# Optimization experiments

Measured on AMD Instinct MI355X. Metric: run time of the kernel, lower is better.

The kernel has to match this reference:

```python
import jax, jax.numpy as jnp
import numpy as np

LATENT = 292
T = 120          # max_length
CHARSET = 35     # charset_length
B = 512
H1, H2, H3 = 701, 701, 901


def _p(key, shape, scale=0.05):
    return jax.random.normal(key, shape, dtype=jnp.float32) * scale


def setup_inputs() -> dict:
    key = jax.random.key(0)
    ks = jax.random.split(key, 12)
    z32 = lambda *s: jnp.zeros(s, jnp.float32)
    return {
        "z": jax.random.normal(ks[0], (B, LATENT), dtype=jnp.float32),
        # linear_1: Dense(latent_dim, selu)
        "W1": _p(ks[1], (LATENT, LATENT)), "b1": z32(LATENT),
        # gru_1 (Keras GRU, reset_after=True): kernel [in,3H], recurrent [H,3H], two bias vectors [3H]
        "gWi1": _p(ks[2], (LATENT, 3 * H1)), "gWh1": _p(ks[3], (H1, 3 * H1)),
        "gbi1": z32(3 * H1), "gbh1": z32(3 * H1),
        # gru_2
        "gWi2": _p(ks[4], (H1, 3 * H2)), "gWh2": _p(ks[5], (H2, 3 * H2)),
        "gbi2": z32(3 * H2), "gbh2": z32(3 * H2),
        # gru_3
        "gWi3": _p(ks[6], (H2, 3 * H3)), "gWh3": _p(ks[7], (H3, 3 * H3)),
        "gbi3": z32(3 * H3), "gbh3": z32(3 * H3),
        # linear_2: TimeDistributed(Dense(charset_length))
        "Wo": _p(ks[8], (H3, CHARSET)), "bo": z32(CHARSET),
    }


def _gru(x_seq, Wi, Wh, bi, bh):
    """Keras GRU (reset_after=True, gate order z,r,h), return_sequences=True.
    x_seq: [B,T,D] -> [B,T,H]. Input projections hoisted out of the scan."""
    H = Wh.shape[0]
    bsz = x_seq.shape[0]
    xp = jnp.einsum('btd,dg->btg', x_seq, Wi) + bi  # [B,T,3H]
    xp = jnp.transpose(xp, (1, 0, 2))               # [T,B,3H] for scan
    h0 = jnp.zeros((bsz, H), x_seq.dtype)

    def step(h, xt):
        rp = h @ Wh + bh                             # recurrent projection [B,3H]
        xz, xr, xh = jnp.split(xt, 3, axis=-1)
        rz, rr, rh = jnp.split(rp, 3, axis=-1)
        zg = jax.nn.sigmoid(xz + rz)
        rg = jax.nn.sigmoid(xr + rr)
        hh = jnp.tanh(xh + rg * rh)                  # reset applied after recurrent matmul
        hn = zg * h + (1.0 - zg) * hh
        return hn, hn

    _, ys = jax.lax.scan(step, h0, xp)               # ys: [T,B,H]
    return jnp.transpose(ys, (1, 0, 2))


def reference(z, W1, b1, gWi1, gWh1, gbi1, gbh1, gWi2, gWh2, gbi2, gbh2,
              gWi3, gWh3, gbi3, gbh3, Wo, bo):
    x = jax.nn.selu(z @ W1 + b1)                             # [B,latent]
    xs = jnp.broadcast_to(x[:, None, :], (x.shape[0], T, x.shape[1]))  # RepeatVector
    h = _gru(xs, gWi1, gWh1, gbi1, gbh1)                     # [B,T,701]
    h = _gru(h, gWi2, gWh2, gbi2, gbh2)                      # [B,T,701] (dropout inactive at inference)
    h = _gru(h, gWi3, gWh3, gbi3, gbh3)                      # [B,T,901]
    logits = jnp.einsum('bth,hc->btc', h, Wo) + bo           # [B,T,charset]
    return jax.nn.softmax(logits, axis=2)
```

## Files before the change

kernel.cpp:

```cpp
#include <hip/hip_runtime.h>
#include <hip/hip_bf16.h>
#include <math.h>

typedef unsigned short u16;
typedef __attribute__((ext_vector_type(4))) float f32x4;
typedef __attribute__((ext_vector_type(8))) short s16x8;

#define BB  512
#define TT  120
#define LAT 292
#define HH1 701
#define HH3 901
#define H1P 704
#define H3P 960
#define CH  35

static const size_t O_X    = 0;
static const size_t O_XP1  = 598016;
static const size_t O_H1F  = 4923392;
static const size_t O_H2F  = 7806976;
static const size_t O_H3F  = 10690560;
static const size_t O_H1B  = 14622720;
static const size_t O_H2B  = 16064512;
static const size_t O_H3B  = 17506304;
static const size_t O_WHT1 = 19472384;
static const size_t O_WIT2 = 22446080;
static const size_t O_WHT2 = 25419776;
static const size_t O_WIT3 = 28393472;
static const size_t O_WHT3 = 32358400;
static const size_t O_WOT  = 37765120;
static const size_t O_TAB  = 37888000;
static const size_t ZERO_BYTES = 14548992;

#define DSWZ(row, g) ((((g) ^ ((row) & 7)) << 4))

static __device__ __forceinline__ u16 f2b(float f){
  union { float f; unsigned int i; } v; v.f = f;
  unsigned int x = v.i;
  return (u16)((x + 0x7FFFu + ((x >> 16) & 1u)) >> 16);
}

#define GLL16(g, l) __builtin_amdgcn_global_load_lds( \
    (const __attribute__((address_space(1))) unsigned int*)(g), \
    (__attribute__((address_space(3))) unsigned int*)(l), 16, 0, 0)

__launch_bounds__(256)
__global__ void k_selu(const float* __restrict__ z, const float* __restrict__ W1,
                       const float* __restrict__ b1, float* __restrict__ x)
{
  int idx = blockIdx.x * 256 + threadIdx.x;
  if (idx >= BB * LAT) return;
  int b = idx / LAT, i = idx - b * LAT;
  float acc = b1[i];
  const float* zr = z + (size_t)b * LAT;
  for (int k = 0; k < LAT; ++k)
    acc += zr[k] * W1[k * LAT + i];
  const float alpha = 1.6732632423543772f, scale = 1.0507009873554805f;
  x[idx] = scale * (acc > 0.f ? acc : alpha * (expf(acc) - 1.f));
}

__launch_bounds__(256)
__global__ void k_xp1(const float* __restrict__ x, const float* __restrict__ Wi1,
                      const float* __restrict__ bi1, float* __restrict__ xp1)
{
  int nb = blockIdx.x % 9, bb = blockIdx.x / 9;
  int n = nb * 256 + threadIdx.x;
  int b0 = bb * 8;
  if (n >= 2112) return;
  if (n >= 2103) { for (int r = 0; r < 8; ++r) xp1[(size_t)(b0 + r) * 2112 + n] = 0.f; return; }
  float bias = bi1[n];
  float acc[8];
  for (int r = 0; r < 8; ++r) acc[r] = bias;
  for (int k = 0; k < LAT; ++k) {
    float w = Wi1[(size_t)k * 2103 + n];
    #pragma unroll
    for (int r = 0; r < 8; ++r) acc[r] += x[(size_t)(b0 + r) * LAT + k] * w;
  }
  for (int r = 0; r < 8; ++r) xp1[(size_t)(b0 + r) * 2112 + n] = acc[r];
}

__launch_bounds__(256)
__global__ void k_transpose(const float* __restrict__ W, u16* __restrict__ WT,
                            int K, int N, int Kpad, int RowsPad)
{
  int tilesN = RowsPad / 64;
  int tk = blockIdx.x / tilesN, tn = blockIdx.x % tilesN;
  int k0 = tk * 64, n0 = tn * 64;
  __shared__ u16 lds[64][72];
  int tid = threadIdx.x;
  int nl = tid & 63, q = tid >> 6;
  for (int i = 0; i < 16; ++i) {
    int kl = q * 16 + i;
    int k = k0 + kl, n = n0 + nl;
    lds[kl][nl] = (k < K && n < N) ? f2b(W[(size_t)k * N + n]) : (u16)0;
  }
  __syncthreads();
  for (int i = 0; i < 16; ++i) {
    int rl = q * 16 + i;
    WT[(size_t)(n0 + rl) * Kpad + k0 + nl] = lds[nl][rl];
  }
}

__global__ void k_maketab(unsigned int* __restrict__ tab)
{
  if (threadIdx.x != 0 || blockIdx.x != 0) return;
  for (int x = 0; x < 8; ++x) {
    for (int li = 0; li < 32; ++li) {
      unsigned v;
      if (li < 15) {
        int t3 = 15 * x + li;
        v = 0xFFFF0000u | (2u << 12) | ((unsigned)(t3 & 7) << 8) | (unsigned)(t3 >> 3);
      } else if (li < 26) {
        int t2 = 11 * x + (li - 15);
        v = 0xFFFF0000u | (1u << 12) | ((unsigned)(t2 & 7) << 8) | (unsigned)(t2 >> 3);
      } else if (li < 31) {
        int pi = 5 * x + (li - 26);
        int i0 = 2 * pi, i1 = 2 * pi + 1;
        unsigned lo = ((unsigned)(i0 & 7) << 8) | (unsigned)(i0 >> 3);
        unsigned hw = ((unsigned)(i1 & 7) << 8) | (unsigned)(i1 >> 3);
        v = lo | (hw << 16);
      } else {
        if (x < 4) {
          unsigned lo = (3u << 12) | ((unsigned)(2 * x) << 8);
          unsigned hw = (3u << 12) | ((unsigned)(2 * x + 1) << 8);
          v = lo | (hw << 16);
        } else {
          int pi = 40 + (x - 4);
          int i0 = 2 * pi, i1 = 2 * pi + 1;
          unsigned lo = ((unsigned)(i0 & 7) << 8) | (unsigned)(i0 >> 3);
          unsigned hw = ((unsigned)(i1 & 7) << 8) | (unsigned)(i1 >> 3);
          v = lo | (hw << 16);
        }
      }
      tab[x + 8 * li] = v;
    }
  }
}


static __device__ __forceinline__ void stage_gru(
    const u16* __restrict__ A, int As, const u16* __restrict__ W, int Ws, int WH,
    int r0, int j0, int kbase, int wl, int lane, char* buf)
{
  #pragma unroll
  for (int i = 0; i < 8; ++i) {
    int slot = wl * 512 + i * 64 + lane;
    const u16* g;
    if (slot < 512) {
      int row = slot >> 3, gl = slot & 7;
      int gq = gl ^ (row & 7);
      g = A + (size_t)(r0 + row) * As + kbase + gq * 8;
    } else {
      int s2 = slot - 512;
      int gate = s2 >> 9, loc = s2 & 511;
      int col = loc >> 3, gl = loc & 7;
      int gq = gl ^ (col & 7);
      g = W + ((size_t)gate * WH + j0 + col) * Ws + kbase + gq * 8;
    }
    char* l = buf + (wl * 512 + i * 64) * 16;
    GLL16(g, l);
  }
}

template<int HACC>
static __device__ __forceinline__ void mm_gru(const char* gb, int wr, int wc, int m16, int kg,
                                              f32x4 (&acc)[4][2][2])
{
  #pragma unroll
  for (int s = 0; s < 2; ++s) {
    s16x8 af[2];
    #pragma unroll
    for (int fm = 0; fm < 2; ++fm) {
      int row = wr * 32 + fm * 16 + m16;
      af[fm] = *(const s16x8*)(gb + row * 128 + DSWZ(row, s * 4 + kg));
    }
    #pragma unroll
    for (int g = 0; g < 3; ++g) {
      #pragma unroll
      for (int fn = 0; fn < 2; ++fn) {
        int col = wc * 32 + fn * 16 + m16;
        s16x8 bf = *(const s16x8*)(gb + 8192 + g * 8192 + col * 128 + DSWZ(col, s * 4 + kg));
        const int ai = (g == 2) ? HACC : g;
        #pragma unroll
        for (int fm = 0; fm < 2; ++fm)
          acc[ai][fm][fn] = __builtin_amdgcn_mfma_f32_16x16x32_bf16(af[fm], bf, acc[ai][fm][fn], 0, 0, 0);
      }
    }
  }
}

static __device__ __forceinline__ void gru_pipe(
    const u16* A0, int As0, const u16* W0, int Ws0,
    const u16* A1, int As1, const u16* W1p, int Ws1,
    int WH, int n0, int n1, int k1off,
    int r0, int j0, char* g0, char* g1, int wl, int lane,
    int wr, int wc, int m16, int kg, f32x4 (&acc)[4][2][2])
{
  const int n = n0 + n1;
#define STG(C, BUF) do { int c_ = (C); \
    if (c_ < n0) stage_gru(A0, As0, W0, Ws0, WH, r0, j0, c_ * 64, wl, lane, (BUF)); \
    else         stage_gru(A1, As1, W1p, Ws1, WH, r0, j0, (c_ - n0) * 64 + k1off, wl, lane, (BUF)); \
  } while (0)
  STG(0, g0);
  __syncthreads();
  for (int ch = 0; ch < n; ch += 2) {
    if (ch + 1 < n) STG(ch + 1, g1);
    if (ch < n0) mm_gru<2>(g0, wr, wc, m16, kg, acc);
    else         mm_gru<3>(g0, wr, wc, m16, kg, acc);
    __syncthreads();
    if (ch + 1 >= n) break;
    if (ch + 2 < n) STG(ch + 2, g0);
    if (ch + 1 < n0) mm_gru<2>(g1, wr, wc, m16, kg, acc);
    else             mm_gru<3>(g1, wr, wc, m16, kg, acc);
    __syncthreads();
  }
#undef STG
}

__launch_bounds__(512, 2)
__global__ void k_wave(int s, const unsigned int* __restrict__ tab,
    const u16* __restrict__ WhT1, const u16* __restrict__ WiT2, const u16* __restrict__ WhT2,
    const u16* __restrict__ WiT3, const u16* __restrict__ WhT3, const u16* __restrict__ WoT,
    const float* __restrict__ xp1,
    const float* __restrict__ gbh1,
    const float* __restrict__ gbi2, const float* __restrict__ gbh2,
    const float* __restrict__ gbi3, const float* __restrict__ gbh3,
    const float* __restrict__ bo,
    float* __restrict__ h1f, u16* __restrict__ h1b,
    float* __restrict__ h2f, u16* __restrict__ h2b,
    float* __restrict__ h3f, u16* __restrict__ h3b,
    float* __restrict__ out)
{
  extern __shared__ __align__(16) char smem[];
  const int tid  = threadIdx.x;
  const int wgrp = tid >> 8;
  const int ltid = tid & 255;
  const int lane = tid & 63;
  const int wl   = (tid >> 6) & 3;
  const int wr = wl >> 1, wc = wl & 1;
  const int m16 = lane & 15, kg = lane >> 4;
  char* g0 = smem + wgrp * 65536;
  char* g1 = g0 + 32768;

  const unsigned e  = tab[blockIdx.x];
  const unsigned lo = e & 0xFFFFu, hi = e >> 16;
  const bool ksplit = (hi == 0xFFFFu);
  const unsigned item = (!ksplit && wgrp == 1) ? hi : lo;
  const int L  = (item >> 12) & 3;
  const int rr = (item >> 8) & 0xF;
  const int cc = item & 0xFF;
  const int t = s - L;
  if (t < 0 || t >= TT) return;
  const int cur = s & 1, prv = cur ^ 1;

  if (L == 3) {
    const int r0 = rr * 64;
    const u16* Ab = h3b + (size_t)prv * BB * H3P;
    f32x4 acc2[2][2];
    { f32x4 z4 = {0.f,0.f,0.f,0.f}; for (int a=0;a<2;++a) for (int b=0;b<2;++b) acc2[a][b]=z4; }
    int4 ra[2], rb2[2];
    const int n = H3P / 64;
    #pragma unroll
    for (int it = 0; it < 2; ++it) {
      int gi = it * 256 + ltid; int r = gi >> 3, gq = gi & 7;
      ra[it]  = *(const int4*)(Ab + (size_t)(r0 + r) * H3P + gq * 8);
      rb2[it] = *(const int4*)(WoT + (size_t)r * H3P + gq * 8);
    }
    #pragma unroll
    for (int it = 0; it < 2; ++it) {
      int gi = it * 256 + ltid; int r = gi >> 3, gq = gi & 7;
      *(int4*)(g0 + r * 128 + DSWZ(r, gq)) = ra[it];
      *(int4*)(g0 + 8192 + r * 128 + DSWZ(r, gq)) = rb2[it];
    }
    __syncthreads();
    for (int ch = 0; ch < n; ++ch) {
      const bool have = (ch + 1 < n);
      if (have) {
        int kb = (ch + 1) * 64;
        #pragma unroll
        for (int it = 0; it < 2; ++it) {
          int gi = it * 256 + ltid; int r = gi >> 3, gq = gi & 7;
          ra[it]  = *(const int4*)(Ab + (size_t)(r0 + r) * H3P + kb + gq * 8);
          rb2[it] = *(const int4*)(WoT + (size_t)r * H3P + kb + gq * 8);
        }
      }
      #pragma unroll
      for (int s2 = 0; s2 < 2; ++s2) {
        s16x8 af[2], bf[2];
        #pragma unroll
        for (int fm = 0; fm < 2; ++fm) {
          int row = wr * 32 + fm * 16 + m16;
          af[fm] = *(const s16x8*)(g0 + row * 128 + DSWZ(row, s2 * 4 + kg));
        }
        #pragma unroll
        for (int fn = 0; fn < 2; ++fn) {
          int col = wc * 32 + fn * 16 + m16;
          bf[fn] = *(const s16x8*)(g0 + 8192 + col * 128 + DSWZ(col, s2 * 4 + kg));
        }
        #pragma unroll
        for (int fm = 0; fm < 2; ++fm)
          #pragma unroll
          for (int fn = 0; fn < 2; ++fn)
            acc2[fm][fn] = __builtin_amdgcn_mfma_f32_16x16x32_bf16(af[fm], bf[fn], acc2[fm][fn], 0, 0, 0);
      }
      if (have) {
        __syncthreads();
        #pragma unroll
        for (int it = 0; it < 2; ++it) {
          int gi = it * 256 + ltid; int r = gi >> 3, gq = gi & 7;
          *(int4*)(g0 + r * 128 + DSWZ(r, gq)) = ra[it];
          *(int4*)(g0 + 8192 + r * 128 + DSWZ(r, gq)) = rb2[it];
        }
        __syncthreads();
      }
    }
    __syncthreads();
    float (*ldsL)[68] = (float (*)[68])g0;
    #pragma unroll
    for (int fn = 0; fn < 2; ++fn) {
      int col = wc * 32 + fn * 16 + m16;
      float bov = (col < CH) ? bo[col] : 0.f;
      #pragma unroll
      for (int fm = 0; fm < 2; ++fm)
        #pragma unroll
        for (int ii = 0; ii < 4; ++ii)
          ldsL[wr * 32 + fm * 16 + kg * 4 + ii][col] = acc2[fm][fn][ii] + bov;
    }
    __syncthreads();
    if (ltid < 64) {
      int b = r0 + ltid;
      float mx = -1e30f;
      for (int c2 = 0; c2 < CH; ++c2) mx = fmaxf(mx, ldsL[ltid][c2]);
      float sum = 0.f;
      for (int c2 = 0; c2 < CH; ++c2) sum += expf(ldsL[ltid][c2] - mx);
      float inv = 1.f / sum;
      size_t ob = ((size_t)b * TT + t) * CH;
      for (int c2 = 0; c2 < CH; ++c2) out[ob + c2] = expf(ldsL[ltid][c2] - mx) * inv;
    }
    return;
  }

  int H, HP;
  const u16 *A0 = nullptr, *W0 = nullptr, *A1 = nullptr, *W1p = nullptr;
  int As0 = 0, Ws0 = 0, As1 = 0, Ws1 = 0, n0 = 0, n1 = 0, k1off = 0;
  const float *bi = nullptr, *bh;
  float *hfP, *hfC; u16 *hbC;
  if (L == 0) {
    H = HH1; HP = H1P;
    A1 = h1b + (size_t)prv * BB * H1P; As1 = H1P; W1p = WhT1; Ws1 = H1P; n1 = 11;
    bh = gbh1;
    hfP = h1f + (size_t)prv * BB * H1P; hfC = h1f + (size_t)cur * BB * H1P;
    hbC = h1b + (size_t)cur * BB * H1P;
  } else if (L == 1) {
    H = HH1; HP = H1P;
    bi = gbi2; bh = gbh2;
    hfP = h2f + (size_t)prv * BB * H1P; hfC = h2f + (size_t)cur * BB * H1P;
    hbC = h2b + (size_t)cur * BB * H1P;
    if (wgrp == 0) { A0 = h1b + (size_t)prv * BB * H1P; As0 = H1P; W0 = WiT2; Ws0 = H1P; n0 = 11; }
    else           { A1 = h2b + (size_t)prv * BB * H1P; As1 = H1P; W1p = WhT2; Ws1 = H1P; n1 = 11; }
  } else {
    H = HH3; HP = H3P;
    bi = gbi3; bh = gbh3;
    hfP = h3f + (size_t)prv * BB * H3P; hfC = h3f + (size_t)cur * BB * H3P;
    hbC = h3b + (size_t)cur * BB * H3P;
    if (wgrp == 0) {
      A0 = h2b + (size_t)prv * BB * H1P; As0 = H1P; W0 = WiT3; Ws0 = H1P; n0 = 11;
      A1 = h3b + (size_t)prv * BB * H3P; As1 = H3P; W1p = WhT3; Ws1 = H3P; n1 = 2; k1off = 0;
    } else {
      A1 = h3b + (size_t)prv * BB * H3P; As1 = H3P; W1p = WhT3; Ws1 = H3P; n1 = 13; k1off = 128;
    }
  }
  const int r0 = rr * 64, j0 = cc * 64;

  f32x4 acc[4][2][2];
  {
    f32x4 z4 = {0.f, 0.f, 0.f, 0.f};
    for (int g = 0; g < 4; ++g) for (int a = 0; a < 2; ++a) for (int b = 0; b < 2; ++b) acc[g][a][b] = z4;
  }

  gru_pipe(A0, As0, W0, Ws0, A1, As1, W1p, Ws1, H, n0, n1, k1off,
           r0, j0, g0, g1, wl, lane, wr, wc, m16, kg, acc);

  if (ksplit) {
    __syncthreads();
    float* red = (float*)smem;
    if (wgrp == 1) {
      float* b = red + ltid * 64;
      #pragma unroll
      for (int g = 0; g < 4; ++g)
        #pragma unroll
        for (int fm = 0; fm < 2; ++fm)
          #pragma unroll
          for (int fn = 0; fn < 2; ++fn)
            *(f32x4*)(b + ((g * 2 + fm) * 2 + fn) * 4) = acc[g][fm][fn];
    }
    __syncthreads();
    if (wgrp == 1) return;
    {
      const float* b = red + ltid * 64;
      #pragma unroll
      for (int g = 0; g < 4; ++g)
        #pragma unroll
        for (int fm = 0; fm < 2; ++fm)
          #pragma unroll
          for (int fn = 0; fn < 2; ++fn)
            acc[g][fm][fn] += *(const f32x4*)(b + ((g * 2 + fm) * 2 + fn) * 4);
    }
  }

  #pragma unroll
  for (int fn = 0; fn < 2; ++fn) {
    int j = j0 + wc * 32 + fn * 16 + m16;
    if (j >= H) continue;
    float bhz = bh[j], bhr = bh[H + j], bhh = bh[2 * H + j];
    float biz = 0.f, bir = 0.f, bih = 0.f;
    if (L != 0) { biz = bi[j]; bir = bi[H + j]; bih = bi[2 * H + j]; }
    #pragma unroll
    for (int fm = 0; fm < 2; ++fm) {
      #pragma unroll
      for (int ii = 0; ii < 4; ++ii) {
        int row = r0 + wr * 32 + fm * 16 + kg * 4 + ii;
        float az  = acc[0][fm][fn][ii];
        float ar  = acc[1][fm][fn][ii];
        float axh = acc[2][fm][fn][ii];
        float arh = acc[3][fm][fn][ii];
        float pz, pr, xh_, rh_;
        if (L == 0) {
          const float* xr_ = xp1 + (size_t)row * 2112;
          pz  = xr_[j] + az + bhz;
          pr  = xr_[HH1 + j] + ar + bhr;
          xh_ = xr_[2 * HH1 + j];
          rh_ = arh + bhh;
        } else {
          pz  = az + biz + bhz;
          pr  = ar + bir + bhr;
          xh_ = axh + bih;
          rh_ = arh + bhh;
        }
        float zg = 1.f / (1.f + expf(-pz));
        float rg = 1.f / (1.f + expf(-pr));
        float hh = tanhf(xh_ + rg * rh_);
        float hp = hfP[(size_t)row * HP + j];
        float hn = zg * hp + (1.f - zg) * hh;
        hfC[(size_t)row * HP + j] = hn;
        hbC[(size_t)row * HP + j] = f2b(hn);
      }
    }
  }
}

extern "C" void kernel_launch(void* const* d_in, const int* in_sizes, int n_in,
                              void* d_out, int out_size, void* d_ws, size_t ws_size,
                              hipStream_t stream)
{
  const float* z    = (const float*)d_in[0];
  const float* W1   = (const float*)d_in[1];
  const float* b1   = (const float*)d_in[2];
  const float* gWi1 = (const float*)d_in[3];
  const float* gWh1 = (const float*)d_in[4];
  const float* gbi1 = (const float*)d_in[5];
  const float* gbh1 = (const float*)d_in[6];
  const float* gWi2 = (const float*)d_in[7];
  const float* gWh2 = (const float*)d_in[8];
  const float* gbi2 = (const float*)d_in[9];
  const float* gbh2 = (const float*)d_in[10];
  const float* gWi3 = (const float*)d_in[11];
  const float* gWh3 = (const float*)d_in[12];
  const float* gbi3 = (const float*)d_in[13];
  const float* gbh3 = (const float*)d_in[14];
  const float* Wo   = (const float*)d_in[15];
  const float* bo   = (const float*)d_in[16];

  char* ws = (char*)d_ws;
  float* x_f  = (float*)(ws + O_X);
  float* xp1  = (float*)(ws + O_XP1);
  float* h1f  = (float*)(ws + O_H1F);
  float* h2f  = (float*)(ws + O_H2F);
  float* h3f  = (float*)(ws + O_H3F);
  u16*   h1b  = (u16*)(ws + O_H1B);
  u16*   h2b  = (u16*)(ws + O_H2B);
  u16*   h3b  = (u16*)(ws + O_H3B);
  u16*   WhT1 = (u16*)(ws + O_WHT1);
  u16*   WiT2 = (u16*)(ws + O_WIT2);
  u16*   WhT2 = (u16*)(ws + O_WHT2);
  u16*   WiT3 = (u16*)(ws + O_WIT3);
  u16*   WhT3 = (u16*)(ws + O_WHT3);
  u16*   WoT  = (u16*)(ws + O_WOT);
  unsigned int* tab = (unsigned int*)(ws + O_TAB);

  hipFuncSetAttribute((const void*)k_wave,
                      hipFuncAttributeMaxDynamicSharedMemorySize, 131072);

  hipMemsetAsync(ws + O_H1F, 0, ZERO_BYTES, stream);

  k_maketab<<<1, 64, 0, stream>>>(tab);
  k_selu<<<(BB * LAT + 255) / 256, 256, 0, stream>>>(z, W1, b1, x_f);
  k_xp1<<<9 * 64, 256, 0, stream>>>(x_f, gWi1, gbi1, xp1);

  k_transpose<<<11 * 33, 256, 0, stream>>>(gWh1, WhT1, 701, 2103, 704, 2112);
  k_transpose<<<11 * 33, 256, 0, stream>>>(gWi2, WiT2, 701, 2103, 704, 2112);
  k_transpose<<<11 * 33, 256, 0, stream>>>(gWh2, WhT2, 701, 2103, 704, 2112);
  k_transpose<<<11 * 44, 256, 0, stream>>>(gWi3, WiT3, 701, 2703, 704, 2816);
  k_transpose<<<15 * 44, 256, 0, stream>>>(gWh3, WhT3, 901, 2703, 960, 2816);
  k_transpose<<<15 * 1, 256, 0, stream>>>(Wo, WoT, 901, 35, 960, 64);

  for (int s = 0; s < TT + 3; ++s)
    k_wave<<<256, 512, 131072, stream>>>(s, tab, WhT1, WiT2, WhT2, WiT3, WhT3, WoT, xp1,
                                         gbh1, gbi2, gbh2, gbi3, gbh3, bo,
                                         h1f, h1b, h2f, h2b, h3f, h3b, (float*)d_out);
}
```

Measured before the change: 4.983 ms.

## Replace double-buffered K=64 staging with 4-slot K=32 ring and vmcnt waits

```diff
diff --git a/kernel.cpp b/kernel.cpp
--- a/kernel.cpp
+++ b/kernel.cpp
@@ -137,84 +137,78 @@
   }
 }
 
-
-static __device__ __forceinline__ void stage_gru(
+#define RD32(base, row, q) ((base) + (row) * 64 + ((((q) - ((row) >> 2)) & 3) << 4))
+
+static __device__ __forceinline__ void stage32(
     const u16* __restrict__ A, int As, const u16* __restrict__ W, int Ws, int WH,
     int r0, int j0, int kbase, int wl, int lane, char* buf)
 {
   #pragma unroll
-  for (int i = 0; i < 8; ++i) {
-    int slot = wl * 512 + i * 64 + lane;
-    const u16* g;
-    if (slot < 512) {
-      int row = slot >> 3, gl = slot & 7;
-      int gq = gl ^ (row & 7);
-      g = A + (size_t)(r0 + row) * As + kbase + gq * 8;
+  for (int i = 0; i < 4; ++i) {
+    const int si = wl * 4 + i;
+    char* l = buf + si * 1024;
+    if (si < 4) {
+      int slot = si * 64 + lane;
+      int row = slot >> 2, gl = slot & 3;
+      int gq = (gl + (row >> 2)) & 3;
+      GLL16(A + (size_t)(r0 + row) * As + kbase + gq * 8, l);
     } else {
-      int s2 = slot - 512;
-      int gate = s2 >> 9, loc = s2 & 511;
-      int col = loc >> 3, gl = loc & 7;
-      int gq = gl ^ (col & 7);
-      g = W + ((size_t)gate * WH + j0 + col) * Ws + kbase + gq * 8;
-    }
-    char* l = buf + (wl * 512 + i * 64) * 16;
-    GLL16(g, l);
+      int s2 = si * 64 + lane - 256;
+      int gate = s2 >> 8, loc = s2 & 255;
+      int col = loc >> 2, gl = loc & 3;
+      int gq = (gl + (col >> 2)) & 3;
+      GLL16(W + ((size_t)gate * WH + j0 + col) * Ws + kbase + gq * 8, l);
+    }
   }
 }
 
 template<int HACC>
-static __device__ __forceinline__ void mm_gru(const char* gb, int wr, int wc, int m16, int kg,
-                                              f32x4 (&acc)[4][2][2])
-{
+static __device__ __forceinline__ void mm32(const char* gb, int wr, int wc, int m16, int kg,
+                                            f32x4 (&acc)[4][2][2])
+{
+  s16x8 af[2];
   #pragma unroll
-  for (int s = 0; s < 2; ++s) {
-    s16x8 af[2];
+  for (int fm = 0; fm < 2; ++fm) {
+    int row = wr * 32 + fm * 16 + m16;
+    af[fm] = *(const s16x8*)RD32(gb, row, kg);
+  }
+  #pragma unroll
+  for (int g = 0; g < 3; ++g) {
     #pragma unroll
-    for (int fm = 0; fm < 2; ++fm) {
-      int row = wr * 32 + fm * 16 + m16;
-      af[fm] = *(const s16x8*)(gb + row * 128 + DSWZ(row, s * 4 + kg));
-    }
-    #pragma unroll
-    for (int g = 0; g < 3; ++g) {
+    for (int fn = 0; fn < 2; ++fn) {
+      int col = wc * 32 + fn * 16 + m16;
+      s16x8 bf = *(const s16x8*)RD32(gb + 4096 + g * 4096, col, kg);
+      const int ai = (g == 2) ? HACC : g;
       #pragma unroll
-      for (int fn = 0; fn < 2; ++fn) {
-        int col = wc * 32 + fn * 16 + m16;
-        s16x8 bf = *(const s16x8*)(gb + 8192 + g * 8192 + col * 128 + DSWZ(col, s * 4 + kg));
-        const int ai = (g == 2) ? HACC : g;
-        #pragma unroll
-        for (int fm = 0; fm < 2; ++fm)
-          acc[ai][fm][fn] = __builtin_amdgcn_mfma_f32_16x16x32_bf16(af[fm], bf, acc[ai][fm][fn], 0, 0, 0);
-      }
-    }
-  }
-}
-
-static __device__ __forceinline__ void gru_pipe(
+      for (int fm = 0; fm < 2; ++fm)
+        acc[ai][fm][fn] = __builtin_amdgcn_mfma_f32_16x16x32_bf16(af[fm], bf, acc[ai][fm][fn], 0, 0, 0);
+    }
+  }
+}
+
+static __device__ __forceinline__ void gru_pipe32(
     const u16* A0, int As0, const u16* W0, int Ws0,
     const u16* A1, int As1, const u16* W1p, int Ws1,
     int WH, int n0, int n1, int k1off,
-    int r0, int j0, char* g0, char* g1, int wl, int lane,
+    int r0, int j0, char* ring, int wl, int lane,
     int wr, int wc, int m16, int kg, f32x4 (&acc)[4][2][2])
 {
   const int n = n0 + n1;
-#define STG(C, BUF) do { int c_ = (C); \
-    if (c_ < n0) stage_gru(A0, As0, W0, Ws0, WH, r0, j0, c_ * 64, wl, lane, (BUF)); \
-    else         stage_gru(A1, As1, W1p, Ws1, WH, r0, j0, (c_ - n0) * 64 + k1off, wl, lane, (BUF)); \
+#define STG32(C) do { int c_ = (C); char* b_ = ring + (c_ & 3) * 16384; \
+    if (c_ < n0) stage32(A0, As0, W0, Ws0, WH, r0, j0, c_ * 32, wl, lane, b_); \
+    else         stage32(A1, As1, W1p, Ws1, WH, r0, j0, (c_ - n0) * 32 + k1off, wl, lane, b_); \
   } while (0)
-  STG(0, g0);
-  __syncthreads();
-  for (int ch = 0; ch < n; ch += 2) {
-    if (ch + 1 < n) STG(ch + 1, g1);
-    if (ch < n0) mm_gru<2>(g0, wr, wc, m16, kg, acc);
-    else         mm_gru<3>(g0, wr, wc, m16, kg, acc);
-    __syncthreads();
-    if (ch + 1 >= n) break;
-    if (ch + 2 < n) STG(ch + 2, g0);
-    if (ch + 1 < n0) mm_gru<2>(g1, wr, wc, m16, kg, acc);
-    else             mm_gru<3>(g1, wr, wc, m16, kg, acc);
-    __syncthreads();
-  }
-#undef STG
+  STG32(0); STG32(1); STG32(2);
+  for (int ch = 0; ch < n; ++ch) {
+    if (ch + 2 < n)      asm volatile("s_waitcnt vmcnt(8)" ::: "memory");
+    else if (ch + 1 < n) asm volatile("s_waitcnt vmcnt(4)" ::: "memory");
+    else                 asm volatile("s_waitcnt vmcnt(0)" ::: "memory");
+    __builtin_amdgcn_s_barrier();
+    if (ch + 3 < n) STG32(ch + 3);
+    if (ch < n0) mm32<2>(ring + (ch & 3) * 16384, wr, wc, m16, kg, acc);
+    else         mm32<3>(ring + (ch & 3) * 16384, wr, wc, m16, kg, acc);
+  }
+#undef STG32
 }
 
 __launch_bounds__(512, 2)
@@ -239,8 +233,7 @@
   const int wl   = (tid >> 6) & 3;
   const int wr = wl >> 1, wc = wl & 1;
   const int m16 = lane & 15, kg = lane >> 4;
-  char* g0 = smem + wgrp * 65536;
-  char* g1 = g0 + 32768;
+  char* ring = smem + wgrp * 65536;
 
   const unsigned e  = tab[blockIdx.x];
   const unsigned lo = e & 0xFFFFu, hi = e >> 16;
@@ -254,6 +247,7 @@
   const int cur = s & 1, prv = cur ^ 1;
 
   if (L == 3) {
+    char* g0 = ring;
     const int r0 = rr * 64;
     const u16* Ab = h3b + (size_t)prv * BB * H3P;
     f32x4 acc2[2][2];
@@ -347,7 +341,7 @@
   float *hfP, *hfC; u16 *hbC;
   if (L == 0) {
     H = HH1; HP = H1P;
-    A1 = h1b + (size_t)prv * BB * H1P; As1 = H1P; W1p = WhT1; Ws1 = H1P; n1 = 11;
+    A1 = h1b + (size_t)prv * BB * H1P; As1 = H1P; W1p = WhT1; Ws1 = H1P; n1 = 22;
     bh = gbh1;
     hfP = h1f + (size_t)prv * BB * H1P; hfC = h1f + (size_t)cur * BB * H1P;
     hbC = h1b + (size_t)cur * BB * H1P;
@@ -356,18 +350,18 @@
     bi = gbi2; bh = gbh2;
     hfP = h2f + (size_t)prv * BB * H1P; hfC = h2f + (size_t)cur * BB * H1P;
     hbC = h2b + (size_t)cur * BB * H1P;
-    if (wgrp == 0) { A0 = h1b + (size_t)prv * BB * H1P; As0 = H1P; W0 = WiT2; Ws0 = H1P; n0 = 11; }
-    else           { A1 = h2b + (size_t)prv * BB * H1P; As1 = H1P; W1p = WhT2; Ws1 = H1P; n1 = 11; }
+    if (wgrp == 0) { A0 = h1b + (size_t)prv * BB * H1P; As0 = H1P; W0 = WiT2; Ws0 = H1P; n0 = 22; }
+    else           { A1 = h2b + (size_t)prv * BB * H1P; As1 = H1P; W1p = WhT2; Ws1 = H1P; n1 = 22; }
   } else {
     H = HH3; HP = H3P;
     bi = gbi3; bh = gbh3;
     hfP = h3f + (size_t)prv * BB * H3P; hfC = h3f + (size_t)cur * BB * H3P;
     hbC = h3b + (size_t)cur * BB * H3P;
     if (wgrp == 0) {
-      A0 = h2b + (size_t)prv * BB * H1P; As0 = H1P; W0 = WiT3; Ws0 = H1P; n0 = 11;
-      A1 = h3b + (size_t)prv * BB * H3P; As1 = H3P; W1p = WhT3; Ws1 = H3P; n1 = 2; k1off = 0;
+      A0 = h2b + (size_t)prv * BB * H1P; As0 = H1P; W0 = WiT3; Ws0 = H1P; n0 = 22;
+      A1 = h3b + (size_t)prv * BB * H3P; As1 = H3P; W1p = WhT3; Ws1 = H3P; n1 = 4; k1off = 0;
     } else {
-      A1 = h3b + (size_t)prv * BB * H3P; As1 = H3P; W1p = WhT3; Ws1 = H3P; n1 = 13; k1off = 128;
+      A1 = h3b + (size_t)prv * BB * H3P; As1 = H3P; W1p = WhT3; Ws1 = H3P; n1 = 26; k1off = 128;
     }
   }
   const int r0 = rr * 64, j0 = cc * 64;
@@ -378,8 +372,8 @@
     for (int g = 0; g < 4; ++g) for (int a = 0; a < 2; ++a) for (int b = 0; b < 2; ++b) acc[g][a][b] = z4;
   }
 
-  gru_pipe(A0, As0, W0, Ws0, A1, As1, W1p, Ws1, H, n0, n1, k1off,
-           r0, j0, g0, g1, wl, lane, wr, wc, m16, kg, acc);
+  gru_pipe32(A0, As0, W0, Ws0, A1, As1, W1p, Ws1, H, n0, n1, k1off,
+             r0, j0, ring, wl, lane, wr, wc, m16, kg, acc);
 
   if (ksplit) {
     __syncthreads();
```

Result: no change. 5.001 ms (+0.4%).

## Replace per-step kernel launches with persistent kernel using grid barrier and ring buffers

Applied to the files above, without the earlier changes.

```diff
diff --git a/kernel.cpp b/kernel.cpp
--- a/kernel.cpp
+++ b/kernel.cpp
@@ -14,6 +14,7 @@
 #define H1P 704
 #define H3P 960
 #define CH  35
+#define NSTEP (TT + 3)
 
 static const size_t O_X    = 0;
 static const size_t O_XP1  = 598016;
@@ -30,7 +31,12 @@
 static const size_t O_WHT3 = 32358400;
 static const size_t O_WOT  = 37765120;
 static const size_t O_TAB  = 37888000;
-static const size_t ZERO_BYTES = 14548992;
+static const size_t O_CNT  = 37889024;
+static const size_t ZERO_SMALL = 14548992;
+static const size_t RING_BASE  = 37900288;
+static const size_t S1B = (size_t)BB * H1P * 2;
+static const size_t S3B = (size_t)BB * H3P * 2;
+static const size_t SLOTALL = S1B + S1B + S3B;
 
 #define DSWZ(row, g) ((((g) ^ ((row) & 7)) << 4))
 
@@ -43,6 +49,10 @@
 #define GLL16(g, l) __builtin_amdgcn_global_load_lds( \
     (const __attribute__((address_space(1))) unsigned int*)(g), \
     (__attribute__((address_space(3))) unsigned int*)(l), 16, 0, 0)
+
+static __device__ __forceinline__ void st_u16_sc(u16* p, u16 v) {
+  asm volatile("global_store_short %0, %1, off sc0 sc1" :: "v"(p), "v"((unsigned)v) : "memory");
+}
 
 __launch_bounds__(256)
 __global__ void k_selu(const float* __restrict__ z, const float* __restrict__ W1,
@@ -63,9 +73,13 @@
 __global__ void k_xp1(const float* __restrict__ x, const float* __restrict__ Wi1,
                       const float* __restrict__ bi1, float* __restrict__ xp1)
 {
+  __shared__ float xs[8][LAT];
   int nb = blockIdx.x % 9, bb = blockIdx.x / 9;
   int n = nb * 256 + threadIdx.x;
   int b0 = bb * 8;
+  for (int i = threadIdx.x; i < 8 * LAT; i += 256)
+    xs[i / LAT][i % LAT] = x[(size_t)(b0 + i / LAT) * LAT + (i % LAT)];
+  __syncthreads();
   if (n >= 2112) return;
   if (n >= 2103) { for (int r = 0; r < 8; ++r) xp1[(size_t)(b0 + r) * 2112 + n] = 0.f; return; }
   float bias = bi1[n];
@@ -74,7 +88,7 @@
   for (int k = 0; k < LAT; ++k) {
     float w = Wi1[(size_t)k * 2103 + n];
     #pragma unroll
-    for (int r = 0; r < 8; ++r) acc[r] += x[(size_t)(b0 + r) * LAT + k] * w;
+    for (int r = 0; r < 8; ++r) acc[r] += xs[r][k] * w;
   }
   for (int r = 0; r < 8; ++r) xp1[(size_t)(b0 + r) * 2112 + n] = acc[r];
 }
@@ -137,7 +151,6 @@
   }
 }
 
-
 static __device__ __forceinline__ void stage_gru(
     const u16* __restrict__ A, int As, const u16* __restrict__ W, int Ws, int WH,
     int r0, int j0, int kbase, int wl, int lane, char* buf)
@@ -217,8 +230,96 @@
 #undef STG
 }
 
+static __device__ __forceinline__ void out_tile(
+    const u16* __restrict__ Ab, const u16* __restrict__ WoT, const float* __restrict__ bo,
+    float* __restrict__ out, int r0, int t,
+    char* g0, int ltid, int wr, int wc, int m16, int kg)
+{
+  f32x4 acc2[2][2];
+  { f32x4 z4 = {0.f,0.f,0.f,0.f}; for (int a=0;a<2;++a) for (int b=0;b<2;++b) acc2[a][b]=z4; }
+  int4 ra[2], rb2[2];
+  const int n = H3P / 64;
+  #pragma unroll
+  for (int it = 0; it < 2; ++it) {
+    int gi = it * 256 + ltid; int r = gi >> 3, gq = gi & 7;
+    ra[it]  = *(const int4*)(Ab + (size_t)(r0 + r) * H3P + gq * 8);
+    rb2[it] = *(const int4*)(WoT + (size_t)r * H3P + gq * 8);
+  }
+  #pragma unroll
+  for (int it = 0; it < 2; ++it) {
+    int gi = it * 256 + ltid; int r = gi >> 3, gq = gi & 7;
+    *(int4*)(g0 + r * 128 + DSWZ(r, gq)) = ra[it];
+    *(int4*)(g0 + 8192 + r * 128 + DSWZ(r, gq)) = rb2[it];
+  }
+  __syncthreads();
+  for (int ch = 0; ch < n; ++ch) {
+    const bool have = (ch + 1 < n);
+    if (have) {
+      int kb = (ch + 1) * 64;
+      #pragma unroll
+      for (int it = 0; it < 2; ++it) {
+        int gi = it * 256 + ltid; int r = gi >> 3, gq = gi & 7;
+        ra[it]  = *(const int4*)(Ab + (size_t)(r0 + r) * H3P + kb + gq * 8);
+        rb2[it] = *(const int4*)(WoT + (size_t)r * H3P + kb + gq * 8);
+      }
+    }
+    #pragma unroll
+    for (int s2 = 0; s2 < 2; ++s2) {
+      s16x8 af[2], bf[2];
+      #pragma unroll
+      for (int fm = 0; fm < 2; ++fm) {
+        int row = wr * 32 + fm * 16 + m16;
+        af[fm] = *(const s16x8*)(g0 + row * 128 + DSWZ(row, s2 * 4 + kg));
+      }
+      #pragma unroll
+      for (int fn = 0; fn < 2; ++fn) {
+        int col = wc * 32 + fn * 16 + m16;
+        bf[fn] = *(const s16x8*)(g0 + 8192 + col * 128 + DSWZ(col, s2 * 4 + kg));
+      }
+      #pragma unroll
+      for (int fm = 0; fm < 2; ++fm)
+        #pragma unroll
+        for (int fn = 0; fn < 2; ++fn)
+          acc2[fm][fn] = __builtin_amdgcn_mfma_f32_16x16x32_bf16(af[fm], bf[fn], acc2[fm][fn], 0, 0, 0);
+    }
+    if (have) {
+      __syncthreads();
+      #pragma unroll
+      for (int it = 0; it < 2; ++it) {
+        int gi = it * 256 + ltid; int r = gi >> 3, gq = gi & 7;
+        *(int4*)(g0 + r * 128 + DSWZ(r, gq)) = ra[it];
+        *(int4*)(g0 + 8192 + r * 128 + DSWZ(r, gq)) = rb2[it];
+      }
+      __syncthreads();
+    }
+  }
+  __syncthreads();
+  float (*ldsL)[68] = (float (*)[68])g0;
+  #pragma unroll
+  for (int fn = 0; fn < 2; ++fn) {
+    int col = wc * 32 + fn * 16 + m16;
+    float bov = (col < CH) ? bo[col] : 0.f;
+    #pragma unroll
+    for (int fm = 0; fm < 2; ++fm)
+      #pragma unroll
+      for (int ii = 0; ii < 4; ++ii)
+        ldsL[wr * 32 + fm * 16 + kg * 4 + ii][col] = acc2[fm][fn][ii] + bov;
+  }
+  __syncthreads();
+  if (ltid < 64) {
+    int b = r0 + ltid;
+    float mx = -1e30f;
+    for (int c2 = 0; c2 < CH; ++c2) mx = fmaxf(mx, ldsL[ltid][c2]);
+    float sum = 0.f;
+    for (int c2 = 0; c2 < CH; ++c2) sum += expf(ldsL[ltid][c2] - mx);
+    float inv = 1.f / sum;
+    size_t ob = ((size_t)b * TT + t) * CH;
+    for (int c2 = 0; c2 < CH; ++c2) out[ob + c2] = expf(ldsL[ltid][c2] - mx) * inv;
+  }
+}
+
 __launch_bounds__(512, 2)
-__global__ void k_wave(int s, const unsigned int* __restrict__ tab,
+__global__ void k_wave9(int s, const unsigned int* __restrict__ tab,
     const u16* __restrict__ WhT1, const u16* __restrict__ WiT2, const u16* __restrict__ WhT2,
     const u16* __restrict__ WiT3, const u16* __restrict__ WhT3, const u16* __restrict__ WoT,
     const float* __restrict__ xp1,
@@ -254,113 +355,29 @@
   const int cur = s & 1, prv = cur ^ 1;
 
   if (L == 3) {
-    const int r0 = rr * 64;
-    const u16* Ab = h3b + (size_t)prv * BB * H3P;
-    f32x4 acc2[2][2];
-    { f32x4 z4 = {0.f,0.f,0.f,0.f}; for (int a=0;a<2;++a) for (int b=0;b<2;++b) acc2[a][b]=z4; }
-    int4 ra[2], rb2[2];
-    const int n = H3P / 64;
-    #pragma unroll
-    for (int it = 0; it < 2; ++it) {
-      int gi = it * 256 + ltid; int r = gi >> 3, gq = gi & 7;
-      ra[it]  = *(const int4*)(Ab + (size_t)(r0 + r) * H3P + gq * 8);
-      rb2[it] = *(const int4*)(WoT + (size_t)r * H3P + gq * 8);
-    }
-    #pragma unroll
-    for (int it = 0; it < 2; ++it) {
-      int gi = it * 256 + ltid; int r = gi >> 3, gq = gi & 7;
-      *(int4*)(g0 + r * 128 + DSWZ(r, gq)) = ra[it];
-      *(int4*)(g0 + 8192 + r * 128 + DSWZ(r, gq)) = rb2[it];
-    }
-    __syncthreads();
-    for (int ch = 0; ch < n; ++ch) {
-      const bool have = (ch + 1 < n);
-      if (have) {
-        int kb = (ch + 1) * 64;
-        #pragma unroll
-        for (int it = 0; it < 2; ++it) {
-          int gi = it * 256 + ltid; int r = gi >> 3, gq = gi & 7;
-          ra[it]  = *(const int4*)(Ab + (size_t)(r0 + r) * H3P + kb + gq * 8);
-          rb2[it] = *(const int4*)(WoT + (size_t)r * H3P + kb + gq * 8);
-        }
-      }
-      #pragma unroll
-      for (int s2 = 0; s2 < 2; ++s2) {
-        s16x8 af[2], bf[2];
-        #pragma unroll
-        for (int fm = 0; fm < 2; ++fm) {
-          int row = wr * 32 + fm * 16 + m16;
-          af[fm] = *(const s16x8*)(g0 + row * 128 + DSWZ(row, s2 * 4 + kg));
-        }
-        #pragma unroll
-        for (int fn = 0; fn < 2; ++fn) {
-          int col = wc * 32 + fn * 16 + m16;
-          bf[fn] = *(const s16x8*)(g0 + 8192 + col * 128 + DSWZ(col, s2 * 4 + kg));
-        }
-        #pragma unroll
-        for (int fm = 0; fm < 2; ++fm)
-          #pragma unroll
-          for (int fn = 0; fn < 2; ++fn)
-            acc2[fm][fn] = __builtin_amdgcn_mfma_f32_16x16x32_bf16(af[fm], bf[fn], acc2[fm][fn], 0, 0, 0);
-      }
-      if (have) {
-        __syncthreads();
-        #pragma unroll
-        for (int it = 0; it < 2; ++it) {
-          int gi = it * 256 + ltid; int r = gi >> 3, gq = gi & 7;
-          *(int4*)(g0 + r * 128 + DSWZ(r, gq)) = ra[it];
-          *(int4*)(g0 + 8192 + r * 128 + DSWZ(r, gq)) = rb2[it];
-        }
-        __syncthreads();
-      }
-    }
-    __syncthreads();
-    float (*ldsL)[68] = (float (*)[68])g0;
-    #pragma unroll
-    for (int fn = 0; fn < 2; ++fn) {
-      int col = wc * 32 + fn * 16 + m16;
-      float bov = (col < CH) ? bo[col] : 0.f;
-      #pragma unroll
-      for (int fm = 0; fm < 2; ++fm)
-        #pragma unroll
-        for (int ii = 0; ii < 4; ++ii)
-          ldsL[wr * 32 + fm * 16 + kg * 4 + ii][col] = acc2[fm][fn][ii] + bov;
-    }
-    __syncthreads();
-    if (ltid < 64) {
-      int b = r0 + ltid;
-      float mx = -1e30f;
-      for (int c2 = 0; c2 < CH; ++c2) mx = fmaxf(mx, ldsL[ltid][c2]);
-      float sum = 0.f;
-      for (int c2 = 0; c2 < CH; ++c2) sum += expf(ldsL[ltid][c2] - mx);
-      float inv = 1.f / sum;
-      size_t ob = ((size_t)b * TT + t) * CH;
-      for (int c2 = 0; c2 < CH; ++c2) out[ob + c2] = expf(ldsL[ltid][c2] - mx) * inv;
-    }
+    out_tile(h3b + (size_t)prv * BB * H3P, WoT, bo, out, rr * 64, t, g0, ltid, wr, wc, m16, kg);
     return;
   }
 
-  int H, HP;
+  int H;
   const u16 *A0 = nullptr, *W0 = nullptr, *A1 = nullptr, *W1p = nullptr;
   int As0 = 0, Ws0 = 0, As1 = 0, Ws1 = 0, n0 = 0, n1 = 0, k1off = 0;
   const float *bi = nullptr, *bh;
   float *hfP, *hfC; u16 *hbC;
   if (L == 0) {
-    H = HH1; HP = H1P;
+    H = HH1;
     A1 = h1b + (size_t)prv * BB * H1P; As1 = H1P; W1p = WhT1; Ws1 = H1P; n1 = 11;
     bh = gbh1;
     hfP = h1f + (size_t)prv * BB * H1P; hfC = h1f + (size_t)cur * BB * H1P;
     hbC = h1b + (size_t)cur * BB * H1P;
   } else if (L == 1) {
-    H = HH1; HP = H1P;
-    bi = gbi2; bh = gbh2;
+    H = HH1; bi = gbi2; bh = gbh2;
     hfP = h2f + (size_t)prv * BB * H1P; hfC = h2f + (size_t)cur * BB * H1P;
     hbC = h2b + (size_t)cur * BB * H1P;
-    if (wgrp == 0) { A0 = h1b + (size_t)prv * BB * H1P; As0 = H1P; W0 = WiT2; Ws0 = H1P; n0 = 11; }
+    if (wgrp == 0) { A0 = h1b + (size_t)prv * BB * H1P; As0 = H1P; W0 = WiT2; Ws0 = H1P; n0 = 11; As1 = H1P; }
     else           { A1 = h2b + (size_t)prv * BB * H1P; As1 = H1P; W1p = WhT2; Ws1 = H1P; n1 = 11; }
   } else {
-    H = HH3; HP = H3P;
-    bi = gbi3; bh = gbh3;
+    H = HH3; bi = gbi3; bh = gbh3;
     hfP = h3f + (size_t)prv * BB * H3P; hfC = h3f + (size_t)cur * BB * H3P;
     hbC = h3b + (size_t)cur * BB * H3P;
     if (wgrp == 0) {
@@ -373,10 +390,8 @@
   const int r0 = rr * 64, j0 = cc * 64;
 
   f32x4 acc[4][2][2];
-  {
-    f32x4 z4 = {0.f, 0.f, 0.f, 0.f};
-    for (int g = 0; g < 4; ++g) for (int a = 0; a < 2; ++a) for (int b = 0; b < 2; ++b) acc[g][a][b] = z4;
-  }
+  { f32x4 z4 = {0.f, 0.f, 0.f, 0.f};
+    for (int g = 0; g < 4; ++g) for (int a = 0; a < 2; ++a) for (int b = 0; b < 2; ++b) acc[g][a][b] = z4; }
 
   gru_pipe(A0, As0, W0, Ws0, A1, As1, W1p, Ws1, H, n0, n1, k1off,
            r0, j0, g0, g1, wl, lane, wr, wc, m16, kg, acc);
@@ -440,11 +455,179 @@
         float zg = 1.f / (1.f + expf(-pz));
         float rg = 1.f / (1.f + expf(-pr));
         float hh = tanhf(xh_ + rg * rh_);
-        float hp = hfP[(size_t)row * HP + j];
+        float hp = hfP[(size_t)row * As1 + j];
         float hn = zg * hp + (1.f - zg) * hh;
-        hfC[(size_t)row * HP + j] = hn;
-        hbC[(size_t)row * HP + j] = f2b(hn);
-      }
+        hfC[(size_t)row * As1 + j] = hn;
+        hbC[(size_t)row * As1 + j] = f2b(hn);
+      }
+    }
+  }
+}
+
+__launch_bounds__(512, 2)
+__global__ void k_pers(int s0, int s1, int R,
+    const unsigned int* __restrict__ tab, unsigned int* __restrict__ cnt,
+    const u16* __restrict__ WhT1, const u16* __restrict__ WiT2, const u16* __restrict__ WhT2,
+    const u16* __restrict__ WiT3, const u16* __restrict__ WhT3, const u16* __restrict__ WoT,
+    const float* __restrict__ xp1,
+    const float* __restrict__ gbh1,
+    const float* __restrict__ gbi2, const float* __restrict__ gbh2,
+    const float* __restrict__ gbi3, const float* __restrict__ gbh3,
+    const float* __restrict__ bo,
+    u16* __restrict__ h1r, u16* __restrict__ h2r, u16* __restrict__ h3r,
+    float* __restrict__ h1f, float* __restrict__ h2f, float* __restrict__ h3f,
+    float* __restrict__ out)
+{
+  extern __shared__ __align__(16) char smem[];
+  const int tid  = threadIdx.x;
+  const int wgrp = tid >> 8;
+  const int ltid = tid & 255;
+  const int lane = tid & 63;
+  const int wl   = (tid >> 6) & 3;
+  const int wr = wl >> 1, wc = wl & 1;
+  const int m16 = lane & 15, kg = lane >> 4;
+  char* g0 = smem + wgrp * 65536;
+  char* g1 = g0 + 32768;
+
+  const unsigned e  = tab[blockIdx.x];
+  const unsigned lo = e & 0xFFFFu, hi = e >> 16;
+  const bool ksplit = (hi == 0xFFFFu);
+  const unsigned item = (!ksplit && wgrp == 1) ? hi : lo;
+  const int L  = (item >> 12) & 3;
+  const int rr = (item >> 8) & 0xF;
+  const int cc = item & 0xFF;
+  const int r0 = rr * 64, j0 = cc * 64;
+
+  int H = 0, As0 = 0, Ws0 = 0, As1 = H3P, Ws1 = 0, n0 = 0, n1 = 0, k1off = 0;
+  const u16 *A0base = nullptr, *W0p = nullptr, *A1base = nullptr, *W1p = nullptr;
+  u16 *hbCbase = nullptr;
+  float *hfbase = nullptr;
+  const float *bi = nullptr, *bh = nullptr;
+  bool do_epi = false;
+  if (L == 0) {
+    H = HH1;
+    A1base = h1r; As1 = H1P; W1p = WhT1; Ws1 = H1P; n1 = 11;
+    bh = gbh1; hbCbase = h1r; hfbase = h1f; do_epi = true;
+  } else if (L == 1) {
+    H = HH1; bi = gbi2; bh = gbh2; hbCbase = h2r; hfbase = h2f;
+    As1 = H1P;
+    if (wgrp == 0) { A0base = h1r; As0 = H1P; W0p = WiT2; Ws0 = H1P; n0 = 11; do_epi = true; }
+    else           { A1base = h2r; W1p = WhT2; Ws1 = H1P; n1 = 11; }
+  } else if (L == 2) {
+    H = HH3; bi = gbi3; bh = gbh3; hbCbase = h3r; hfbase = h3f;
+    As1 = H3P;
+    if (wgrp == 0) {
+      A0base = h2r; As0 = H1P; W0p = WiT3; Ws0 = H1P; n0 = 11;
+      A1base = h3r; W1p = WhT3; Ws1 = H3P; n1 = 2; k1off = 0; do_epi = true;
+    } else {
+      A1base = h3r; W1p = WhT3; Ws1 = H3P; n1 = 13; k1off = 128;
+    }
+  }
+
+  for (int s = s0; s < s1; ++s) {
+    const int t = s - L;
+    const int cur2 = s & 1, prv2 = cur2 ^ 1;
+    const int curS = s % R, prvS = (s + R - 1) % R;
+
+    if (t >= 0 && t < TT) {
+      if (L == 3) {
+        out_tile(h3r + (size_t)prvS * BB * H3P, WoT, bo, out, r0, t, g0, ltid, wr, wc, m16, kg);
+      } else {
+        const u16* A0 = A0base ? A0base + (size_t)prvS * BB * As0 : nullptr;
+        const u16* A1 = A1base ? A1base + (size_t)prvS * BB * As1 : nullptr;
+
+        f32x4 acc[4][2][2];
+        { f32x4 z4 = {0.f,0.f,0.f,0.f};
+          for (int g = 0; g < 4; ++g) for (int a = 0; a < 2; ++a) for (int b = 0; b < 2; ++b) acc[g][a][b] = z4; }
+
+        gru_pipe(A0, As0, W0p, Ws0, A1, As1, W1p, Ws1, H, n0, n1, k1off,
+                 r0, j0, g0, g1, wl, lane, wr, wc, m16, kg, acc);
+
+        if (ksplit) {
+          __syncthreads();
+          float* red = (float*)smem;
+          if (wgrp == 1) {
+            float* b = red + ltid * 64;
+            #pragma unroll
+            for (int g = 0; g < 4; ++g)
+              #pragma unroll
+              for (int fm = 0; fm < 2; ++fm)
+                #pragma unroll
+                for (int fn = 0; fn < 2; ++fn)
+                  *(f32x4*)(b + ((g * 2 + fm) * 2 + fn) * 4) = acc[g][fm][fn];
+          }
+          __syncthreads();
+          if (wgrp == 0) {
+            const float* b = red + ltid * 64;
+            #pragma unroll
+            for (int g = 0; g < 4; ++g)
+              #pragma unroll
+              for (int fm = 0; fm < 2; ++fm)
+                #pragma unroll
+                for (int fn = 0; fn < 2; ++fn)
+                  acc[g][fm][fn] += *(const f32x4*)(b + ((g * 2 + fm) * 2 + fn) * 4);
+          }
+        }
+
+        if (do_epi) {
+          float* hfP = hfbase + (size_t)prv2 * BB * As1;
+          float* hfC = hfbase + (size_t)cur2 * BB * As1;
+          u16* hbC = hbCbase + (size_t)curS * BB * As1;
+          #pragma unroll
+          for (int fn = 0; fn < 2; ++fn) {
+            int j = j0 + wc * 32 + fn * 16 + m16;
+            if (j >= H) continue;
+            float bhz = bh[j], bhr = bh[H + j], bhh = bh[2 * H + j];
+            float biz = 0.f, bir = 0.f, bih = 0.f;
+            if (L != 0) { biz = bi[j]; bir = bi[H + j]; bih = bi[2 * H + j]; }
+            #pragma unroll
+            for (int fm = 0; fm < 2; ++fm) {
+              #pragma unroll
+              for (int ii = 0; ii < 4; ++ii) {
+                int row = r0 + wr * 32 + fm * 16 + kg * 4 + ii;
+                float az  = acc[0][fm][fn][ii];
+                float ar  = acc[1][fm][fn][ii];
+                float axh = acc[2][fm][fn][ii];
+                float arh = acc[3][fm][fn][ii];
+                float pz, pr, xh_, rh_;
+                if (L == 0) {
+                  const float* xr_ = xp1 + (size_t)row * 2112;
+                  pz  = xr_[j] + az + bhz;
+                  pr  = xr_[HH1 + j] + ar + bhr;
+                  xh_ = xr_[2 * HH1 + j];
+                  rh_ = arh + bhh;
+                } else {
+                  pz  = az + biz + bhz;
+                  pr  = ar + bir + bhr;
+                  xh_ = axh + bih;
+                  rh_ = arh + bhh;
+                }
+                float zg = 1.f / (1.f + expf(-pz));
+                float rg = 1.f / (1.f + expf(-pr));
+                float hh = tanhf(xh_ + rg * rh_);
+                float hp = hfP[(size_t)row * As1 + j];
+                float hn = zg * hp + (1.f - zg) * hh;
+                hfC[(size_t)row * As1 + j] = hn;
+                st_u16_sc(&hbC[(size_t)row * As1 + j], f2b(hn));
+              }
+            }
+          }
+        }
+      }
+    }
+
+    if (s + 1 < s1) {
+      asm volatile("s_waitcnt vmcnt(0)" ::: "memory");
+      __syncthreads();
+      if (tid == 0) {
+        atomicAdd(&cnt[s], 1u);
+        int guard = 0;
+        while (__hip_atomic_load(&cnt[s], __ATOMIC_RELAXED, __HIP_MEMORY_SCOPE_AGENT) < 256u) {
+          __builtin_amdgcn_s_sleep(2);
+          if (++guard > (1 << 18)) break;
+        }
+      }
+      __syncthreads();
     }
   }
 }
@@ -477,9 +660,6 @@
   float* h1f  = (float*)(ws + O_H1F);
   float* h2f  = (float*)(ws + O_H2F);
   float* h3f  = (float*)(ws + O_H3F);
-  u16*   h1b  = (u16*)(ws + O_H1B);
-  u16*   h2b  = (u16*)(ws + O_H2B);
-  u16*   h3b  = (u16*)(ws + O_H3B);
   u16*   WhT1 = (u16*)(ws + O_WHT1);
   u16*   WiT2 = (u16*)(ws + O_WIT2);
   u16*   WhT2 = (u16*)(ws + O_WHT2);
@@ -487,11 +667,16 @@
   u16*   WhT3 = (u16*)(ws + O_WHT3);
   u16*   WoT  = (u16*)(ws + O_WOT);
   unsigned int* tab = (unsigned int*)(ws + O_TAB);
-
-  hipFuncSetAttribute((const void*)k_wave,
+  unsigned int* cnt = (unsigned int*)(ws + O_CNT);
+
+  hipFuncSetAttribute((const void*)k_pers,
                       hipFuncAttributeMaxDynamicSharedMemorySize, 131072);
-
-  hipMemsetAsync(ws + O_H1F, 0, ZERO_BYTES, stream);
+  hipFuncSetAttribute((const void*)k_wave9,
+                      hipFuncAttributeMaxDynamicSharedMemorySize, 131072);
+
+  size_t avail = (ws_size > RING_BASE) ? (ws_size - RING_BASE) : 0;
+  int R = (int)(avail / SLOTALL);
+  if (R > NSTEP) R = NSTEP;
 
   k_maketab<<<1, 64, 0, stream>>>(tab);
   k_selu<<<(BB * LAT + 255) / 256, 256, 0, stream>>>(z, W1, b1, x_f);
@@ -504,8 +689,32 @@
   k_transpose<<<15 * 44, 256, 0, stream>>>(gWh3, WhT3, 901, 2703, 960, 2816);
   k_transpose<<<15 * 1, 256, 0, stream>>>(Wo, WoT, 901, 35, 960, 64);
 
-  for (int s = 0; s < TT + 3; ++s)
-    k_wave<<<256, 512, 131072, stream>>>(s, tab, WhT1, WiT2, WhT2, WiT3, WhT3, WoT, xp1,
-                                         gbh1, gbi2, gbh2, gbi3, gbh3, bo,
-                                         h1f, h1b, h2f, h2b, h3f, h3b, (float*)d_out);
-}
+  if (R >= 8) {
+    u16* h1r = (u16*)(ws + RING_BASE);
+    u16* h2r = (u16*)(ws + RING_BASE + (size_t)R * S1B);
+    u16* h3r = (u16*)(ws + RING_BASE + (size_t)R * S1B * 2);
+    hipMemsetAsync(ws + O_H1F, 0, ZERO_SMALL, stream);
+    hipMemsetAsync(ws + O_CNT, 0, NSTEP * 4, stream);
+    hipMemsetAsync((char*)h1r + (size_t)(R - 1) * S1B, 0, S1B, stream);
+    hipMemsetAsync((char*)h2r, 0, S1B, stream);
+    hipMemsetAsync((char*)h3r + S3B, 0, S3B, stream);
+    const int G = R - 1;
+    for (int g0 = 0; g0 < NSTEP; g0 += G) {
+      int g1 = g0 + G; if (g1 > NSTEP) g1 = NSTEP;
+      k_pers<<<256, 512, 131072, stream>>>(g0, g1, R, tab, cnt,
+          WhT1, WiT2, WhT2, WiT3, WhT3, WoT, xp1,
+          gbh1, gbi2, gbh2, gbi3, gbh3, bo,
+          h1r, h2r, h3r, h1f, h2f, h3f, (float*)d_out);
+    }
+  } else {
+    u16* h1b = (u16*)(ws + O_H1B);
+    u16* h2b = (u16*)(ws + O_H2B);
+    u16* h3b = (u16*)(ws + O_H3B);
+    hipMemsetAsync(ws + O_H1F, 0, ZERO_SMALL, stream);
+    for (int s = 0; s < NSTEP; ++s)
+      k_wave9<<<256, 512, 131072, stream>>>(s, tab,
+          WhT1, WiT2, WhT2, WiT3, WhT3, WoT, xp1,
+          gbh1, gbi2, gbh2, gbi3, gbh3, bo,
+          h1f, h1b, h2f, h2b, h3f, h3b, (float*)d_out);
+  }
+}
```

Result: slower. 7.414 ms (+48.8%).
